# Performance work log

Measured on AMD Instinct MI355X. Metric: run time of the kernel, lower is better.

The kernel has to match this reference:

```python
import jax, jax.numpy as jnp
import numpy as np


def _bipolarize(x):
    # torchhd.hard_quantize: sign quantize to {-1, +1}
    return jnp.where(x > 0, 1.0, -1.0).astype(x.dtype)


def _transform(am, projections):
    """PQ-HDC Algorithm 1: MAP AM (C,D) -> binary AM (C,P,D) in {0,1} + weights (C,P)."""
    C, D = am.shape

    def per_class(hv):  # hv: (D,)
        bips = []
        loss = hv
        for _ in range(projections):  # P is small (2-4), sequential by construction
            bip = _bipolarize(loss)
            dot = jnp.dot(loss, bip)
            # orthogonal projection of loss onto bip: bip * dot / ||bip||^2
            loss = loss - bip * dot / jnp.sum(bip * bip)
            bips.append(bip)
        X = jnp.stack(bips)  # (P, D) bipolar
        G = X @ X.T  # (P, P)
        w = hv @ X.T @ jnp.linalg.inv(G)  # (P,)
        # normalize: length of w[:,None]*X over full (P,D) matrix
        length = jnp.linalg.norm(w[:, None] * X)
        w = jnp.sqrt(jnp.asarray(D, hv.dtype)) * w / length
        w = w ** 2
        return X, w

    Xs, ws = jax.vmap(per_class)(am)  # (C,P,D), (C,P)
    ambin = jnp.where(Xs > 0, 1.0, 0.0).astype(am.dtype)  # binarize {0,1}
    return ambin, ws


def _phs(qbin, ambin, weights):
    """Pseudo Hamming Similarity, batched. qbin:(B,D) {0,1}; ambin:(C,P,D) {0,1}."""
    D = qbin.shape[-1]
    # equal-bit count = D - sum(q XOR a) = D - sum_q - sum_a + 2*q.a
    dots = jnp.einsum('bd,cpd->bcp', qbin, ambin)  # (B,C,P)
    qsum = jnp.sum(qbin, axis=-1)                  # (B,)
    asum = jnp.sum(ambin, axis=-1)                 # (C,P)
    ham = D - qsum[:, None, None] - asum[None, :, :] + 2.0 * dots
    return jnp.sum(weights[None, :, :] * ham, axis=-1)  # (B,C)


def setup_inputs() -> dict:
    key = jax.random.key(0)
    k1, k2 = jax.random.split(key)
    B, C, D = 4096, 128, 10000
    query = jax.random.normal(k1, (B, D), dtype=jnp.float32)
    am = jax.random.normal(k2, (C, D), dtype=jnp.float32)
    return {"query": query, "am": am, "projections": 3}


def reference(query, am, projections):
    ambin, weights = _transform(am, projections)
    qbin = jnp.where(_bipolarize(query) > 0, 1.0, 0.0).astype(query.dtype)
    return _phs(qbin, ambin, weights)  # (B, C) logits
```

## Files before the change

### kernel.cpp

```cpp
#include <hip/hip_runtime.h>
#include <stdint.h>

typedef unsigned long long u64;

#define D_DIM   10000
#define C_CLS   128
#define WPRP    192
#define NWORDS  160
#define NIT     40
#define GRP     8

__device__ __forceinline__ float wred64(float v) {
#pragma unroll
    for (int m = 1; m <= 32; m <<= 1) v += __shfl_xor(v, m);
    return v;
}
__device__ __forceinline__ int wred64i(int v) {
#pragma unroll
    for (int m = 1; m <= 32; m <<= 1) v += __shfl_xor(v, m);
    return v;
}

__device__ __forceinline__ size_t am_idx(int c, int wi, int p) {
    return ((size_t)c * 32 + (unsigned)wi / 6u) * 18 + (size_t)p * 6 + (unsigned)wi % 6u;
}

__global__ __launch_bounds__(256) void kA_transform(const float* __restrict__ am,
                                                    u64* __restrict__ amw,
                                                    float4* __restrict__ wtab)
{
    const int c = blockIdx.x;
    const int t = threadIdx.x;
    const int w = t >> 6;
    const int l = t & 63;

    __shared__ float redf[4];
    __shared__ int   sI[4][6];
    __shared__ float sF[4][3];

    const float* hvp = am + (size_t)c * D_DIM;

    float4 loss[10], hv[10];
#pragma unroll
    for (int k = 0; k < 10; ++k) {
        const int it = w + 4 * k;
        const int d0 = it * 256 + 4 * l;
        float4 x = make_float4(0.f, 0.f, 0.f, 0.f);
        if (d0 + 3 < D_DIM) x = *(const float4*)(hvp + d0);
        loss[k] = x; hv[k] = x;
    }

    int cnt[3]; float hX[3]; u64 sp[3];

#pragma unroll
    for (int p = 0; p < 3; ++p) {
        float sabs = 0.f;
#pragma unroll
        for (int k = 0; k < 10; ++k)
            sabs += fabsf(loss[k].x) + fabsf(loss[k].y) + fabsf(loss[k].z) + fabsf(loss[k].w);
        sabs = wred64(sabs);
        if (l == 0) redf[w] = sabs;
        __syncthreads();
        const float dot = redf[0] + redf[1] + redf[2] + redf[3];
        __syncthreads();
        const float dd = dot / (float)D_DIM;

        u64 bits = 0; int cc = 0; float hx = 0.f;
#pragma unroll
        for (int k = 0; k < 10; ++k) {
            const int it = w + 4 * k;
            const bool p0 = loss[k].x > 0.f;
            const bool p1 = loss[k].y > 0.f;
            const bool p2 = loss[k].z > 0.f;
            const bool p3 = loss[k].w > 0.f;
            const u64 b0 = __ballot(p0);
            const u64 b1 = __ballot(p1);
            const u64 b2 = __ballot(p2);
            const u64 b3 = __ballot(p3);
            if (l < 4) {
                const u64 bb = (l == 0) ? b0 : ((l == 1) ? b1 : ((l == 2) ? b2 : b3));
                amw[am_idx(c, it * 4 + l, p)] = bb;
            }
            bits |= ((u64)p0 << (4 * k)) | ((u64)p1 << (4 * k + 1))
                  | ((u64)p2 << (4 * k + 2)) | ((u64)p3 << (4 * k + 3));
            cc += (int)p0 + (int)p1 + (int)p2 + (int)p3;
            hx += (p0 ? hv[k].x : -hv[k].x) + (p1 ? hv[k].y : -hv[k].y)
                + (p2 ? hv[k].z : -hv[k].z) + (p3 ? hv[k].w : -hv[k].w);
            float4 L = loss[k];
            L.x -= p0 ? dd : -dd; L.y -= p1 ? dd : -dd;
            L.z -= p2 ? dd : -dd; L.w -= p3 ? dd : -dd;
            const int d0 = it * 256 + 4 * l;
            if (!(d0 + 3 < D_DIM)) L = make_float4(0.f, 0.f, 0.f, 0.f);
            loss[k] = L;
        }
        if (t < WPRP - NWORDS) amw[am_idx(c, NWORDS + t, p)] = 0ull;
        sp[p] = bits; cnt[p] = cc; hX[p] = hx;
    }

    int vi[6] = { cnt[0], cnt[1], cnt[2],
                  static_cast<int>(__popcll(sp[0] ^ sp[1])),
                  static_cast<int>(__popcll(sp[0] ^ sp[2])),
                  static_cast<int>(__popcll(sp[1] ^ sp[2])) };
#pragma unroll
    for (int i = 0; i < 6; ++i) vi[i] = wred64i(vi[i]);
    float vf[3] = { hX[0], hX[1], hX[2] };
#pragma unroll
    for (int i = 0; i < 3; ++i) vf[i] = wred64(vf[i]);
    if (l == 0) {
#pragma unroll
        for (int i = 0; i < 6; ++i) sI[w][i] = vi[i];
#pragma unroll
        for (int i = 0; i < 3; ++i) sF[w][i] = vf[i];
    }
    __syncthreads();
    if (t == 0) {
        int a0 = 0, a1 = 0, a2 = 0, X01 = 0, X02 = 0, X12 = 0;
        float h0f = 0, h1f = 0, h2f = 0;
        for (int i = 0; i < 4; ++i) {
            a0 += sI[i][0]; a1 += sI[i][1]; a2 += sI[i][2];
            X01 += sI[i][3]; X02 += sI[i][4]; X12 += sI[i][5];
            h0f += sF[i][0]; h1f += sF[i][1]; h2f += sF[i][2];
        }
        const double Dv = (double)D_DIM;
        const double h0 = h0f, h1 = h1f, h2 = h2f;
        const double g01 = Dv - 2.0 * X01, g02 = Dv - 2.0 * X02, g12 = Dv - 2.0 * X12;
        const double A00 = Dv * Dv - g12 * g12;
        const double A01 = g02 * g12 - g01 * Dv;
        const double A02 = g01 * g12 - g02 * Dv;
        const double A11 = Dv * Dv - g02 * g02;
        const double A12 = g02 * g01 - Dv * g12;
        const double A22 = Dv * Dv - g01 * g01;
        const double det = Dv * A00 + g01 * A01 + g02 * A02;
        const double w0 = (A00 * h0 + A01 * h1 + A02 * h2) / det;
        const double w1 = (A01 * h0 + A11 * h1 + A12 * h2) / det;
        const double w2 = (A02 * h0 + A12 * h1 + A22 * h2) / det;
        const double s = w0 * w0 + w1 * w1 + w2 * w2;
        const double f0 = w0 * w0 / s, f1 = w1 * w1 / s, f2 = w2 * w2 / s;
        const double cb = -(f0 * a0 + f1 * a1 + f2 * a2);
        wtab[c] = make_float4((float)f0, (float)f1, (float)f2, (float)cb);
    }
}

__global__ __launch_bounds__(256, 4) void kB_phs(const float* __restrict__ query,
                                                 const u64* __restrict__ amw,
                                                 const float4* __restrict__ wtab,
                                                 float* __restrict__ out)
{
    __shared__ u64 qlds[4 * WPRP];
    __shared__ float4 wsh[C_CLS];
    __shared__ float part[4][4][GRP][33];
    const int t = threadIdx.x;
    const int w = t >> 6;
    const int l = t & 63;
    const int r0 = blockIdx.x * 4;

    if (t < C_CLS) wsh[t] = wtab[t];

    {
        const float* qp = query + (size_t)(r0 + w) * D_DIM;
        u64* qrow = qlds + w * WPRP;
        for (int it = 0; it < NIT; ++it) {
            const int d0 = it * 256 + 4 * l;
            float4 x = make_float4(0.f, 0.f, 0.f, 0.f);
            if (d0 + 3 < D_DIM) x = *(const float4*)(qp + d0);
            const u64 b0 = __ballot(x.x > 0.f);
            const u64 b1 = __ballot(x.y > 0.f);
            const u64 b2 = __ballot(x.z > 0.f);
            const u64 b3 = __ballot(x.w > 0.f);
            if (l < 4) qrow[it * 4 + l] = (l == 0) ? b0 : ((l == 1) ? b1 : ((l == 2) ? b2 : b3));
        }
        if (l < 32) qrow[NWORDS + l] = 0ull;
    }
    __syncthreads();

    const int wl = l & 31;
    const int rh = l >> 5;
    const int rA = 2 * rh, rB = 2 * rh + 1;

    const u64* qa = qlds + rA * WPRP + wl * 6;
    const u64* qb = qlds + rB * WPRP + wl * 6;
    const u64 qa0 = qa[0], qa1 = qa[1], qa2 = qa[2], qa3 = qa[3], qa4 = qa[4], qa5 = qa[5];
    const u64 qb0 = qb[0], qb1 = qb[1], qb2 = qb[2], qb3 = qb[3], qb4 = qb[4], qb5 = qb[5];

    const int qsA = (int)(__popcll(qa0) + __popcll(qa1) + __popcll(qa2) +
                          __popcll(qa3) + __popcll(qa4) + __popcll(qa5));
    const int qsB = (int)(__popcll(qb0) + __popcll(qb1) + __popcll(qb2) +
                          __popcll(qb3) + __popcll(qb4) + __popcll(qb5));
    const float offA = 312.5f - (float)qsA;
    const float offB = 312.5f - (float)qsB;

    const int o = l >> 1;
    const int row_loc = o >> 3;
    const int cc = o & 7;
    const int h = l & 1;

    const int c0 = 32 * w;
    float (*pw)[GRP][33] = part[w];

    for (int g = 0; g < 4; ++g) {
        float accA[GRP], accB[GRP];
#pragma unroll
        for (int i = 0; i < GRP; ++i) {
            const int c = c0 + g * GRP + i;
            const u64* ap = amw + ((size_t)c * 32 + wl) * 18;
            const ulonglong2 v0 = *(const ulonglong2*)(ap + 0);
            const ulonglong2 v1 = *(const ulonglong2*)(ap + 2);
            const ulonglong2 v2 = *(const ulonglong2*)(ap + 4);
            const ulonglong2 v3 = *(const ulonglong2*)(ap + 6);
            const ulonglong2 v4 = *(const ulonglong2*)(ap + 8);
            const ulonglong2 v5 = *(const ulonglong2*)(ap + 10);
            const ulonglong2 v6 = *(const ulonglong2*)(ap + 12);
            const ulonglong2 v7 = *(const ulonglong2*)(ap + 14);
            const ulonglong2 v8 = *(const ulonglong2*)(ap + 16);

            const int pA0 = (int)(__popcll(qa0 & v0.x) + __popcll(qa1 & v0.y) + __popcll(qa2 & v1.x)
                          + __popcll(qa3 & v1.y) + __popcll(qa4 & v2.x) + __popcll(qa5 & v2.y));
            const int pA1 = (int)(__popcll(qa0 & v3.x) + __popcll(qa1 & v3.y) + __popcll(qa2 & v4.x)
                          + __popcll(qa3 & v4.y) + __popcll(qa4 & v5.x) + __popcll(qa5 & v5.y));
            const int pA2 = (int)(__popcll(qa0 & v6.x) + __popcll(qa1 & v6.y) + __popcll(qa2 & v7.x)
                          + __popcll(qa3 & v7.y) + __popcll(qa4 & v8.x) + __popcll(qa5 & v8.y));
            const int pB0 = (int)(__popcll(qb0 & v0.x) + __popcll(qb1 & v0.y) + __popcll(qb2 & v1.x)
                          + __popcll(qb3 & v1.y) + __popcll(qb4 & v2.x) + __popcll(qb5 & v2.y));
            const int pB1 = (int)(__popcll(qb0 & v3.x) + __popcll(qb1 & v3.y) + __popcll(qb2 & v4.x)
                          + __popcll(qb3 & v4.y) + __popcll(qb4 & v5.x) + __popcll(qb5 & v5.y));
            const int pB2 = (int)(__popcll(qb0 & v6.x) + __popcll(qb1 & v6.y) + __popcll(qb2 & v7.x)
                          + __popcll(qb3 & v7.y) + __popcll(qb4 & v8.x) + __popcll(qb5 & v8.y));

            const float4 wv = wsh[c];
            const float cw = wv.w * 0.03125f;
            accA[i] = fmaf(2.f, wv.x * (float)pA0 + wv.y * (float)pA1 + wv.z * (float)pA2,
                           offA + cw);
            accB[i] = fmaf(2.f, wv.x * (float)pB0 + wv.y * (float)pB1 + wv.z * (float)pB2,
                           offB + cw);
        }

#pragma unroll
        for (int i = 0; i < GRP; ++i) {
            pw[rA][i][wl] = accA[i];
            pw[rB][i][wl] = accB[i];
        }
        __syncthreads();

        float s = 0.f;
#pragma unroll
        for (int j = 0; j < 16; ++j) s += pw[row_loc][cc][h * 16 + j];
        s += __shfl_xor(s, 1);
        if (h == 0)
            out[(size_t)(r0 + row_loc) * C_CLS + (c0 + g * GRP + cc)] = s;
        __syncthreads();
    }
}

extern "C" void kernel_launch(void* const* d_in, const int* in_sizes, int n_in,
                              void* d_out, int out_size, void* d_ws, size_t ws_size,
                              hipStream_t stream)
{
    const float* query = (const float*)d_in[0];
    const float* am    = (const float*)d_in[1];
    float* out = (float*)d_out;

    float4* wtab = (float4*)d_ws;
    u64* amw = (u64*)((char*)d_ws + 2048);

    const int B = in_sizes[0] / D_DIM;

    hipLaunchKernelGGL(kA_transform, dim3(C_CLS), dim3(256), 0, stream, am, amw, wtab);
    hipLaunchKernelGGL(kB_phs, dim3(B / 4), dim3(256), 0, stream, query, amw, wtab, out);
}
```

Baseline: 96.82 us.

## Double-buffer AM word loads and drop block barriers in per-wave reduction

Each thread now keeps two register batches of binary-AM words. It loads the next class's words while computing popcounts for the current one, and issues the first batch before query binarization. The two __syncthreads around the partial-sum stage are removed, since each wave only touches its own slice of shared memory and can rely on in-order execution within the wave. This aims to hide global/L2 load latency and cut barrier stalls. The cost is more register pressure under the 256x4 launch bounds, which could cause spills.

```diff
diff --git a/kernel.cpp b/kernel.cpp
--- a/kernel.cpp
+++ b/kernel.cpp
@@ -141,6 +141,15 @@
     }
 }
 
+struct AmBatch { ulonglong2 v[9]; };
+
+__device__ __forceinline__ void amload(AmBatch& b, const u64* __restrict__ amw,
+                                       int c, int wl) {
+    const u64* ap = amw + ((size_t)c * 32 + wl) * 18;
+#pragma unroll
+    for (int i = 0; i < 9; ++i) b.v[i] = *(const ulonglong2*)(ap + 2 * i);
+}
+
 __global__ __launch_bounds__(256, 4) void kB_phs(const float* __restrict__ query,
                                                  const u64* __restrict__ amw,
                                                  const float4* __restrict__ wtab,
@@ -153,8 +162,13 @@
     const int w = t >> 6;
     const int l = t & 63;
     const int r0 = blockIdx.x * 4;
+    const int wl = l & 31;
+    const int c0 = 32 * w;
 
     if (t < C_CLS) wsh[t] = wtab[t];
+
+    AmBatch P, N;
+    amload(P, amw, c0, wl);
 
     {
         const float* qp = query + (size_t)(r0 + w) * D_DIM;
@@ -173,19 +187,18 @@
     }
     __syncthreads();
 
-    const int wl = l & 31;
     const int rh = l >> 5;
     const int rA = 2 * rh, rB = 2 * rh + 1;
 
-    const u64* qa = qlds + rA * WPRP + wl * 6;
-    const u64* qb = qlds + rB * WPRP + wl * 6;
-    const u64 qa0 = qa[0], qa1 = qa[1], qa2 = qa[2], qa3 = qa[3], qa4 = qa[4], qa5 = qa[5];
-    const u64 qb0 = qb[0], qb1 = qb[1], qb2 = qb[2], qb3 = qb[3], qb4 = qb[4], qb5 = qb[5];
-
-    const int qsA = (int)(__popcll(qa0) + __popcll(qa1) + __popcll(qa2) +
-                          __popcll(qa3) + __popcll(qa4) + __popcll(qa5));
-    const int qsB = (int)(__popcll(qb0) + __popcll(qb1) + __popcll(qb2) +
-                          __popcll(qb3) + __popcll(qb4) + __popcll(qb5));
+    const u64* qaP = qlds + rA * WPRP + wl * 6;
+    const u64* qbP = qlds + rB * WPRP + wl * 6;
+    u64 qa[6], qb[6];
+#pragma unroll
+    for (int i = 0; i < 6; ++i) { qa[i] = qaP[i]; qb[i] = qbP[i]; }
+
+    int qsA = 0, qsB = 0;
+#pragma unroll
+    for (int i = 0; i < 6; ++i) { qsA += (int)__popcll(qa[i]); qsB += (int)__popcll(qb[i]); }
     const float offA = 312.5f - (float)qsA;
     const float offB = 312.5f - (float)qsB;
 
@@ -194,44 +207,48 @@
     const int cc = o & 7;
     const int h = l & 1;
 
-    const int c0 = 32 * w;
     float (*pw)[GRP][33] = part[w];
 
     for (int g = 0; g < 4; ++g) {
+        const int cbase = c0 + g * GRP;
         float accA[GRP], accB[GRP];
 #pragma unroll
-        for (int i = 0; i < GRP; ++i) {
-            const int c = c0 + g * GRP + i;
-            const u64* ap = amw + ((size_t)c * 32 + wl) * 18;
-            const ulonglong2 v0 = *(const ulonglong2*)(ap + 0);
-            const ulonglong2 v1 = *(const ulonglong2*)(ap + 2);
-            const ulonglong2 v2 = *(const ulonglong2*)(ap + 4);
-            const ulonglong2 v3 = *(const ulonglong2*)(ap + 6);
-            const ulonglong2 v4 = *(const ulonglong2*)(ap + 8);
-            const ulonglong2 v5 = *(const ulonglong2*)(ap + 10);
-            const ulonglong2 v6 = *(const ulonglong2*)(ap + 12);
-            const ulonglong2 v7 = *(const ulonglong2*)(ap + 14);
-            const ulonglong2 v8 = *(const ulonglong2*)(ap + 16);
-
-            const int pA0 = (int)(__popcll(qa0 & v0.x) + __popcll(qa1 & v0.y) + __popcll(qa2 & v1.x)
-                          + __popcll(qa3 & v1.y) + __popcll(qa4 & v2.x) + __popcll(qa5 & v2.y));
-            const int pA1 = (int)(__popcll(qa0 & v3.x) + __popcll(qa1 & v3.y) + __popcll(qa2 & v4.x)
-                          + __popcll(qa3 & v4.y) + __popcll(qa4 & v5.x) + __popcll(qa5 & v5.y));
-            const int pA2 = (int)(__popcll(qa0 & v6.x) + __popcll(qa1 & v6.y) + __popcll(qa2 & v7.x)
-                          + __popcll(qa3 & v7.y) + __popcll(qa4 & v8.x) + __popcll(qa5 & v8.y));
-            const int pB0 = (int)(__popcll(qb0 & v0.x) + __popcll(qb1 & v0.y) + __popcll(qb2 & v1.x)
-                          + __popcll(qb3 & v1.y) + __popcll(qb4 & v2.x) + __popcll(qb5 & v2.y));
-            const int pB1 = (int)(__popcll(qb0 & v3.x) + __popcll(qb1 & v3.y) + __popcll(qb2 & v4.x)
-                          + __popcll(qb3 & v4.y) + __popcll(qb4 & v5.x) + __popcll(qb5 & v5.y));
-            const int pB2 = (int)(__popcll(qb0 & v6.x) + __popcll(qb1 & v6.y) + __popcll(qb2 & v7.x)
-                          + __popcll(qb3 & v7.y) + __popcll(qb4 & v8.x) + __popcll(qb5 & v8.y));
-
-            const float4 wv = wsh[c];
-            const float cw = wv.w * 0.03125f;
-            accA[i] = fmaf(2.f, wv.x * (float)pA0 + wv.y * (float)pA1 + wv.z * (float)pA2,
-                           offA + cw);
-            accB[i] = fmaf(2.f, wv.x * (float)pB0 + wv.y * (float)pB1 + wv.z * (float)pB2,
-                           offB + cw);
+        for (int ii = 0; ii < 4; ++ii) {
+            const int c = cbase + 2 * ii;
+            amload(N, amw, c + 1, wl);
+            {
+                int pA[3] = {0, 0, 0}, pB[3] = {0, 0, 0};
+#pragma unroll
+                for (int p = 0; p < 3; ++p)
+#pragma unroll
+                    for (int j = 0; j < 3; ++j) {
+                        const ulonglong2 vv = P.v[p * 3 + j];
+                        pA[p] += (int)(__popcll(qa[2 * j] & vv.x) + __popcll(qa[2 * j + 1] & vv.y));
+                        pB[p] += (int)(__popcll(qb[2 * j] & vv.x) + __popcll(qb[2 * j + 1] & vv.y));
+                    }
+                const float4 wv = wsh[c];
+                const float cw = wv.w * 0.03125f;
+                accA[2 * ii] = fmaf(2.f, wv.x * (float)pA[0] + wv.y * (float)pA[1] + wv.z * (float)pA[2], offA + cw);
+                accB[2 * ii] = fmaf(2.f, wv.x * (float)pB[0] + wv.y * (float)pB[1] + wv.z * (float)pB[2], offB + cw);
+            }
+            int c2 = c + 2;
+            if (c2 > c0 + 31) c2 = c0;
+            amload(P, amw, c2, wl);
+            {
+                int pA[3] = {0, 0, 0}, pB[3] = {0, 0, 0};
+#pragma unroll
+                for (int p = 0; p < 3; ++p)
+#pragma unroll
+                    for (int j = 0; j < 3; ++j) {
+                        const ulonglong2 vv = N.v[p * 3 + j];
+                        pA[p] += (int)(__popcll(qa[2 * j] & vv.x) + __popcll(qa[2 * j + 1] & vv.y));
+                        pB[p] += (int)(__popcll(qb[2 * j] & vv.x) + __popcll(qb[2 * j + 1] & vv.y));
+                    }
+                const float4 wv = wsh[c + 1];
+                const float cw = wv.w * 0.03125f;
+                accA[2 * ii + 1] = fmaf(2.f, wv.x * (float)pA[0] + wv.y * (float)pA[1] + wv.z * (float)pA[2], offA + cw);
+                accB[2 * ii + 1] = fmaf(2.f, wv.x * (float)pB[0] + wv.y * (float)pB[1] + wv.z * (float)pB[2], offB + cw);
+            }
         }
 
 #pragma unroll
@@ -239,15 +256,12 @@
             pw[rA][i][wl] = accA[i];
             pw[rB][i][wl] = accB[i];
         }
-        __syncthreads();
-
         float s = 0.f;
 #pragma unroll
         for (int j = 0; j < 16; ++j) s += pw[row_loc][cc][h * 16 + j];
         s += __shfl_xor(s, 1);
         if (h == 0)
-            out[(size_t)(r0 + row_loc) * C_CLS + (c0 + g * GRP + cc)] = s;
-        __syncthreads();
+            out[(size_t)(r0 + row_loc) * C_CLS + (cbase + cc)] = s;
     }
 }
 
```

Result: slower. 104.6 us (+8.0%).
